# Optimization experiments

Hardware: AMD Instinct MI355X
Metric: run time of the kernel (lower is better)

Reference implementation:

```python
import jax, jax.numpy as jnp
import numpy as np
from jax import lax

N = 50000          # fluid particles
E = 1_600_000      # radius-graph edges (avg degree 32)
F_IN = 4           # fluidFeatures
NB = 8             # n = m = 8 basis functions per axis
K = NB * NB        # 64 total basis functions
SUPPORT = 1.0      # attributes['support']
LAYERS = [32, 64, 64, 2]


def setup_inputs() -> dict:
    key = jax.random.key(0)
    ks = jax.random.split(key, 24)
    inp = {
        "fluidPositions": jax.random.uniform(ks[0], (N, 2), jnp.float32),
        "fluidFeatures": jax.random.normal(ks[1], (N, F_IN), jnp.float32),
        "edge_i": jax.random.randint(ks[2], (E,), 0, N),  # receiver
        "edge_j": jax.random.randint(ks[3], (E,), 0, N),  # sender
    }
    # conv in/out channels per RbfNet wiring (boundaryFeatures == 0):
    dims = [(F_IN, LAYERS[0]), (2 * LAYERS[0], LAYERS[1]), (LAYERS[1], LAYERS[2]), (LAYERS[2], LAYERS[3])]
    k = 4
    for idx, (ci, co) in enumerate(dims):
        inp[f"cw{idx}"] = 0.1 * jax.random.normal(ks[k], (K, ci, co), jnp.float32); k += 1
        inp[f"cb{idx}"] = jnp.zeros((co,), jnp.float32)
        inp[f"fw{idx}"] = 0.1 * jax.random.normal(ks[k], (ci, co), jnp.float32); k += 1
        inp[f"fb{idx}"] = jnp.zeros((co,), jnp.float32)
    return inp


def _linear_basis(x, n):
    # hat (linear) RBF basis on n uniformly spaced centers in [-1, 1]
    centers = jnp.linspace(-1.0, 1.0, n, dtype=x.dtype)
    spacing = 2.0 / (n - 1)
    return jnp.maximum(0.0, 1.0 - jnp.abs(x[:, None] - centers[None, :]) / spacing)  # [E, n]


def _edge_basis(pos, ei, ej):
    # fluidEdgeLengths = -(pos[j] - pos[i]) / support, clamped to [-1, 1]
    d = (pos[ei] - pos[ej]) / SUPPORT
    d = jnp.clip(d, -1.0, 1.0)
    mask = ei != ej  # centerIgnore: drop self edges
    d = jnp.where(mask[:, None], d, jnp.array([1.0, 0.0], d.dtype))  # keep atan2 grads finite
    r = jnp.sqrt(jnp.sum(d * d, axis=-1) + 1e-12)
    u = jnp.clip(2.0 * r - 1.0, -1.0, 1.0)          # polar mapping: radius -> [-1, 1]
    v = jnp.arctan2(d[:, 1], d[:, 0]) / jnp.pi       # polar mapping: angle  -> [-1, 1]
    bu = _linear_basis(u, NB)
    bv = _linear_basis(v, NB)
    basis = (bu[:, :, None] * bv[:, None, :]).reshape(ei.shape[0], K)  # separable 2D basis
    return basis * mask[:, None].astype(basis.dtype)


def _rbf_conv(x, ei, ej, basis, W, b):
    # out[i] = sum_{e: dst(e)=i} sum_k basis[e,k] * (x[src(e)] @ W[k]) + b
    xj = x[ej]                           # [E, Cin] neighbor gather
    n_nodes = x.shape[0]
    init = jnp.zeros((n_nodes, W.shape[-1]), x.dtype)
    def body(acc, kw):
        bk, Wk = kw                      # bk: [E], Wk: [Cin, Cout]
        mom = jax.ops.segment_sum(bk[:, None] * xj, ei, num_segments=n_nodes)  # [N, Cin]
        return acc + mom @ Wk, None
    out, _ = lax.scan(body, init, (basis.T, W))
    return out + b


def reference(fluidPositions, fluidFeatures, edge_i, edge_j,
              cw0, cb0, fw0, fb0, cw1, cb1, fw1, fb1,
              cw2, cb2, fw2, fb2, cw3, cb3, fw3, fb3):
    basis = _edge_basis(fluidPositions, edge_i, edge_j)
    # layer 0: dense branch + fluid continuous conv, hstacked
    lin0 = fluidFeatures @ fw0 + fb0
    conv0 = _rbf_conv(fluidFeatures, edge_i, edge_j, basis, cw0, cb0)
    ans = jnp.concatenate([lin0, conv0], axis=1)  # [N, 64]
    # layer 1: features 32 != 64 -> no residual
    a = jax.nn.relu(ans)
    ans = _rbf_conv(a, edge_i, edge_j, basis, cw1, cb1) + a @ fw1 + fb1
    # layer 2: features 64 == 64 -> residual add
    a = jax.nn.relu(ans)
    ans = _rbf_conv(a, edge_i, edge_j, basis, cw2, cb2) + a @ fw2 + fb2 + ans
    # layer 3: features 64 != 2 -> no residual
    a = jax.nn.relu(ans)
    ans = _rbf_conv(a, edge_i, edge_j, basis, cw3, cb3) + a @ fw3 + fb3
    return ans / 128.0
```

## Files before the change

kernel.cpp:

```cpp
#include <hip/hip_runtime.h>
#include <math.h>

typedef _Float16 h8 __attribute__((ext_vector_type(8)));
typedef _Float16 h2 __attribute__((ext_vector_type(2)));
typedef float f32x4 __attribute__((ext_vector_type(4)));
typedef unsigned u32x2 __attribute__((ext_vector_type(2)));
typedef unsigned u32x4 __attribute__((ext_vector_type(4)));

__device__ __forceinline__ float clampf(float x, float lo, float hi) {
    return fminf(fmaxf(x, lo), hi);
}

__global__ void zero_ints(int* __restrict__ p, int n) {
    int i = blockIdx.x * 256 + threadIdx.x;
    if (i < n) p[i] = 0;
}

__global__ void repack_wh(const float* __restrict__ cw, const float* __restrict__ fw,
                          _Float16* __restrict__ Wh) {
    int idx = blockIdx.x * 256 + threadIdx.x;
    int total = 4 * 130 * 512;
    if (idx >= total) return;
    int j8 = idx & 7;
    int l = (idx >> 3) & 63;
    int rest = idx >> 9;
    int s = rest % 130;
    int t = rest / 130;
    int p = s * 32 + ((l >> 4) * 8) + j8;
    int co = t * 16 + (l & 15);
    float v = 0.f;
    if (p < 4096) {
        int tile = p >> 8;
        int g = (p >> 6) & 3;
        int m = (p >> 2) & 15;
        int i = p & 3;
        int mt = tile >> 2;
        int ct = tile & 3;
        int bin = mt * 16 + g * 4 + i;
        int c = ct * 16 + m;
        v = cw[(bin * 64 + c) * 64 + co];
    } else if (p < 4160) {
        v = fw[(p - 4096) * 64 + co];
    }
    Wh[idx] = (_Float16)v;
}

__global__ void repack_wh3(const float* __restrict__ cw, const float* __restrict__ fw,
                           _Float16* __restrict__ Wh) {
    int idx = blockIdx.x * 256 + threadIdx.x;
    int total = 130 * 512;
    if (idx >= total) return;
    int j8 = idx & 7;
    int l = (idx >> 3) & 63;
    int s = idx >> 9;
    int p = s * 32 + ((l >> 4) * 8) + j8;
    int co = l & 15;
    float v = 0.f;
    if (co < 2) {
        if (p < 4096) {
            int tile = p >> 8;
            int g = (p >> 6) & 3;
            int m = (p >> 2) & 15;
            int i = p & 3;
            int mt = tile >> 2;
            int ct = tile & 3;
            int bin = mt * 16 + g * 4 + i;
            int c = ct * 16 + m;
            v = cw[(bin * 64 + c) * 2 + co];
        } else if (p < 4160) {
            v = fw[(p - 4096) * 2 + co];
        }
    }
    Wh[idx] = (_Float16)v;
}

__global__ void repack_w0h(const float* __restrict__ cw0, const float* __restrict__ fw0,
                           _Float16* __restrict__ Wh) {
    int idx = blockIdx.x * 256 + threadIdx.x;
    int total = 4 * 9 * 512;
    if (idx >= total) return;
    int j8 = idx & 7;
    int l = (idx >> 3) & 63;
    int rest = idx >> 9;
    int s = rest % 9;
    int t = rest / 9;
    int p = s * 32 + ((l >> 4) * 8) + j8;
    int co = t * 16 + (l & 15);
    float v = 0.f;
    if (p < 256) {
        int bin = p & 63;
        int c = p >> 6;
        if (co >= 32) v = cw0[(bin * 4 + c) * 32 + (co - 32)];
    } else if (p < 260) {
        int c = p - 256;
        if (co < 32) v = fw0[c * 32 + co];
    }
    Wh[idx] = (_Float16)v;
}

__global__ void edge_hist(const int* __restrict__ ei, const int* __restrict__ ej,
                          int* __restrict__ counts, int E) {
    int e = blockIdx.x * 256 + threadIdx.x;
    if (e >= E) return;
    int i = ei[e], j = ej[e];
    if (i != j) atomicAdd(&counts[i], 1);
}

__global__ __launch_bounds__(1024) void scan_kernel(const int* __restrict__ counts,
                                                    int* __restrict__ offs,
                                                    int* __restrict__ cursor, int N) {
    __shared__ int sums[1024];
    const int t = threadIdx.x;
    const int per = (N + 1023) / 1024;
    const int lo = t * per;
    const int hi = min(lo + per, N);
    int s = 0;
    for (int i = lo; i < hi; ++i) s += counts[i];
    sums[t] = s;
    __syncthreads();
    for (int d = 1; d < 1024; d <<= 1) {
        int v = (t >= d) ? sums[t - d] : 0;
        __syncthreads();
        sums[t] += v;
        __syncthreads();
    }
    int run = (t > 0) ? sums[t - 1] : 0;
    for (int i = lo; i < hi; ++i) {
        offs[i] = run;
        cursor[i] = run;
        run += counts[i];
    }
    if (t == 1023) offs[N] = sums[1023];
}

__global__ void edge_scatter(const int* __restrict__ ei, const int* __restrict__ ej,
                             const float* __restrict__ pos, int* __restrict__ cursor,
                             uint4* __restrict__ csr_all, int E) {
    int e = blockIdx.x * 256 + threadIdx.x;
    if (e >= E) return;
    int i = ei[e], j = ej[e];
    if (i == j) return;
    float dx = clampf(pos[i * 2 + 0] - pos[j * 2 + 0], -1.f, 1.f);
    float dy = clampf(pos[i * 2 + 1] - pos[j * 2 + 1], -1.f, 1.f);
    float r = sqrtf(dx * dx + dy * dy + 1e-12f);
    float u = clampf(2.f * r - 1.f, -1.f, 1.f);
    float v = atan2f(dy, dx) * 0.3183098861837907f;
    float tu = (u + 1.f) * 3.5f;
    float tv = (v + 1.f) * 3.5f;
    int iu = min(6, max(0, (int)floorf(tu)));
    int iv = min(6, max(0, (int)floorf(tv)));
    float fu = clampf(tu - (float)iu, 0.f, 1.f);
    float fv = clampf(tv - (float)iv, 0.f, 1.f);
    bool even = (iu & 1) == 0;
    int rowi0 = even ? iu : iu + 1;
    int rowi1 = even ? iu + 1 : iu;
    float wu0 = even ? (1.f - fu) : fu;
    float wu1 = even ? fu : (1.f - fu);
    float gv = 1.f - fv;
    unsigned a0 = (unsigned)__builtin_bit_cast(unsigned short, (_Float16)(wu0 * gv)) |
                  ((unsigned)__builtin_bit_cast(unsigned short, (_Float16)(wu0 * fv)) << 16);
    unsigned a1 = (unsigned)__builtin_bit_cast(unsigned short, (_Float16)(wu1 * gv)) |
                  ((unsigned)__builtin_bit_cast(unsigned short, (_Float16)(wu1 * fv)) << 16);
    int p = atomicAdd(&cursor[i], 1);
    csr_all[p] = make_uint4(
        (unsigned)j | ((unsigned)(rowi0 >> 1) << 17) | ((unsigned)(rowi1 >> 1) << 19) |
            ((unsigned)iv << 21),
        0u, a0, a1);
}

__device__ __forceinline__ void mom_phase1_64(
    const _Float16* __restrict__ xh, const uint4* __restrict__ csr_all,
    _Float16* Ast, _Float16* Bst, unsigned bst_byte,
    int e0, int e1, int lane, f32x4* acc) {
    const int half = lane >> 5;
    const int el = lane & 31;
    const int q = lane >> 4;
    const int m = lane & 15;
    for (int bs = e0; bs < e1; bs += 32) {
        {
            uint4 z4 = make_uint4(0, 0, 0, 0);
#pragma unroll
            for (int zz = 0; zz < 4; ++zz) ((uint4*)Ast)[zz * 64 + lane] = z4;
        }
        int e = bs + el;
        bool ok = e < e1;
        uint4 ca = csr_all[ok ? e : e0];
        int jme = ok ? (int)(ca.x & 0x1FFFF) : -1;
        {
            int iv = (ca.x >> 21) & 7;
            int rowi = half ? (int)((((ca.x >> 19) & 3) << 1) + 1)
                            : (int)(((ca.x >> 17) & 3) << 1);
            h2 wts = __builtin_bit_cast(h2, half ? ca.w : ca.z);
            if (ok) {
                int bin0 = rowi * 8 + iv;
                int bin1 = bin0 + 1;
                int a0 = bin0 * 32 + (((el >> 3) + (bin0 >> 1)) & 3) * 8 + (el & 7);
                int a1 = bin1 * 32 + (((el >> 3) + (bin1 >> 1)) & 3) * 8 + (el & 7);
                Ast[a0] = wts[0];
                Ast[a1] = wts[1];
            }
        }
#pragma unroll
        for (int it = 0; it < 4; ++it) {
            int ee = it * 8 + (lane >> 3);
            int jj = __shfl(jme, ee);
            int c0 = (lane & 7) * 8;
            uint4 bv = make_uint4(0, 0, 0, 0);
            if (jj >= 0) bv = *(const uint4*)(xh + (size_t)jj * 64 + c0);
            int sub = (ee >> 2) * 4 + (c0 >> 4);
            ((uint4*)Bst)[sub * 8 + (ee & 3) * 2 + ((c0 >> 3) & 1)] = bv;
        }
        h8 af[4];
#pragma unroll
        for (int mt = 0; mt < 4; ++mt) {
            int binr = mt * 16 + m;
            int aoff = binr * 32 + ((q + (binr >> 1)) & 3) * 8;
            af[mt] = *(const h8*)(Ast + aoff);
        }
        unsigned bb = bst_byte + (unsigned)(q * 1024 + m * 8);
        h8 bf[4];
#pragma unroll
        for (int ct = 0; ct < 4; ++ct) {
            u32x2 lo, hi;
            asm volatile("ds_read_b64_tr_b16 %0, %2 offset:%3\n\t"
                         "ds_read_b64_tr_b16 %1, %2 offset:%4"
                         : "=&v"(lo), "=&v"(hi)
                         : "v"(bb), "i"(ct * 128), "i"(ct * 128 + 512)
                         : "memory");
            u32x4 t;
            t[0] = lo[0]; t[1] = lo[1]; t[2] = hi[0]; t[3] = hi[1];
            bf[ct] = __builtin_bit_cast(h8, t);
        }
        asm volatile("s_waitcnt lgkmcnt(0)" ::: "memory");
        __builtin_amdgcn_sched_barrier(0);
        __builtin_amdgcn_s_setprio(1);
#pragma unroll
        for (int mt = 0; mt < 4; ++mt)
#pragma unroll
            for (int ct = 0; ct < 4; ++ct)
                acc[mt * 4 + ct] = __builtin_amdgcn_mfma_f32_16x16x32_f16(
                    af[mt], bf[ct], acc[mt * 4 + ct], 0, 0, 0);
        __builtin_amdgcn_s_setprio(0);
    }
}

__device__ __forceinline__ void mom_writeback_64(const f32x4* acc, _Float16* momrow,
                                                 int lane) {
#pragma unroll
    for (int t = 0; t < 16; ++t) {
        h2 lo = {(_Float16)acc[t][0], (_Float16)acc[t][1]};
        h2 hi = {(_Float16)acc[t][2], (_Float16)acc[t][3]};
        h2* dst = (h2*)(momrow + t * 256 + (lane >> 4) * 64 + (lane & 15) * 4);
        dst[0] = lo;
        dst[1] = hi;
    }
}

template <int MODE>
__global__ __launch_bounds__(1024, 4) void conv64_mfma(
    const _Float16* __restrict__ xh, const float* __restrict__ x32,
    const _Float16* __restrict__ Wh,
    const float* __restrict__ cb, const float* __restrict__ fb,
    const int* __restrict__ offs, const uint4* __restrict__ csr_all,
    float* __restrict__ out32, _Float16* __restrict__ xh_out, int nNodes) {
    constexpr int TM = 16;
    constexpr int KSTEPS = 130;
    constexpr int RSH = 4184;
    extern __shared__ _Float16 smem[];
    const int tid = threadIdx.x;
    const int w = tid >> 6;
    const int lane = tid & 63;
    const int base = blockIdx.x * TM;
    const int n = base + w;

    _Float16* Ast = smem + w * RSH;
    _Float16* Bst = Ast + 2048;
    const unsigned bst_byte = (unsigned)((w * RSH + 2048) * 2);

    f32x4 acc[16] = {{0, 0, 0, 0}, {0, 0, 0, 0}, {0, 0, 0, 0}, {0, 0, 0, 0},
                     {0, 0, 0, 0}, {0, 0, 0, 0}, {0, 0, 0, 0}, {0, 0, 0, 0},
                     {0, 0, 0, 0}, {0, 0, 0, 0}, {0, 0, 0, 0}, {0, 0, 0, 0},
                     {0, 0, 0, 0}, {0, 0, 0, 0}, {0, 0, 0, 0}, {0, 0, 0, 0}};

    if (n < nNodes) {
        mom_phase1_64(xh, csr_all, Ast, Bst, bst_byte, offs[n], offs[n + 1], lane, acc);
        mom_writeback_64(acc, smem + w * RSH, lane);
        smem[w * RSH + 4096 + lane] = xh[(size_t)n * 64 + lane];
    }

    const int s0 = w * 8 + min(w, 2);
    const int s_end = s0 + 8 + (w < 2 ? 1 : 0);
    const int quad = lane >> 4;
    const _Float16* arow = smem + (lane & 15) * RSH;

    const uint4* Bp = (const uint4*)Wh;
    uint4 b0[4], b1[4];
#pragma unroll
    for (int t = 0; t < 4; ++t) {
        b0[t] = Bp[((size_t)t * KSTEPS + s0) * 64 + lane];
        b1[t] = Bp[((size_t)t * KSTEPS + s0 + 1) * 64 + lane];
    }
    __syncthreads();
    f32x4 acc2[4] = {{0, 0, 0, 0}, {0, 0, 0, 0}, {0, 0, 0, 0}, {0, 0, 0, 0}};
    for (int s = s0; s < s_end; ++s) {
        uint4 bq[4];
#pragma unroll
        for (int t = 0; t < 4; ++t) {
            bq[t] = b0[t];
            b0[t] = b1[t];
            if (s + 2 < s_end) b1[t] = Bp[((size_t)t * KSTEPS + s + 2) * 64 + lane];
        }
        h8 a = *(const h8*)(arow + s * 32 + quad * 8);
#pragma unroll
        for (int t = 0; t < 4; ++t)
            acc2[t] = __builtin_amdgcn_mfma_f32_16x16x32_f16(a, __builtin_bit_cast(h8, bq[t]),
                                                             acc2[t], 0, 0, 0);
    }
    __syncthreads();
    f32x4* red = (f32x4*)smem;
#pragma unroll
    for (int t = 0; t < 4; ++t) red[(w * 4 + t) * 64 + lane] = acc2[t];
    __syncthreads();
    if (w < 4) {
        f32x4 s = {0, 0, 0, 0};
#pragma unroll
        for (int g = 0; g < 16; ++g) s += red[(g * 4 + w) * 64 + lane];
        const int co = w * 16 + (lane & 15);
#pragma unroll
        for (int i = 0; i < 4; ++i) {
            int nn = base + quad * 4 + i;
            if (nn < nNodes) {
                float res = s[i] + cb[co] + fb[co];
                if (MODE == 2) res += x32[(size_t)nn * 64 + co];
                if (MODE == 1) out32[(size_t)nn * 64 + co] = res;
                xh_out[(size_t)nn * 64 + co] = (_Float16)fmaxf(res, 0.f);
            }
        }
    }
}

__global__ __launch_bounds__(1024, 4) void conv_last_mfma(
    const _Float16* __restrict__ xh, const _Float16* __restrict__ Wh3,
    const float* __restrict__ cb3, const float* __restrict__ fb3,
    const int* __restrict__ offs, const uint4* __restrict__ csr_all,
    float* __restrict__ out, int nNodes) {
    constexpr int TM = 16;
    constexpr int RSH = 4184;
    extern __shared__ _Float16 smem[];
    const int tid = threadIdx.x;
    const int w = tid >> 6;
    const int lane = tid & 63;
    const int base = blockIdx.x * TM;
    const int n = base + w;

    _Float16* Ast = smem + w * RSH;
    _Float16* Bst = Ast + 2048;
    const unsigned bst_byte = (unsigned)((w * RSH + 2048) * 2);

    f32x4 acc[16] = {{0, 0, 0, 0}, {0, 0, 0, 0}, {0, 0, 0, 0}, {0, 0, 0, 0},
                     {0, 0, 0, 0}, {0, 0, 0, 0}, {0, 0, 0, 0}, {0, 0, 0, 0},
                     {0, 0, 0, 0}, {0, 0, 0, 0}, {0, 0, 0, 0}, {0, 0, 0, 0},
                     {0, 0, 0, 0}, {0, 0, 0, 0}, {0, 0, 0, 0}, {0, 0, 0, 0}};

    if (n < nNodes) {
        mom_phase1_64(xh, csr_all, Ast, Bst, bst_byte, offs[n], offs[n + 1], lane, acc);
        mom_writeback_64(acc, smem + w * RSH, lane);
        smem[w * RSH + 4096 + lane] = xh[(size_t)n * 64 + lane];
    }

    const int s0 = w * 8 + min(w, 2);
    const int s_end = s0 + 8 + (w < 2 ? 1 : 0);
    const int quad = lane >> 4;
    const _Float16* arow = smem + (lane & 15) * RSH;
    const uint4* Bp = (const uint4*)Wh3;

    __syncthreads();
    f32x4 acc2 = {0, 0, 0, 0};
    for (int s = s0; s < s_end; ++s) {
        uint4 bq = Bp[(size_t)s * 64 + lane];
        h8 a = *(const h8*)(arow + s * 32 + quad * 8);
        acc2 = __builtin_amdgcn_mfma_f32_16x16x32_f16(a, __builtin_bit_cast(h8, bq),
                                                      acc2, 0, 0, 0);
    }
    __syncthreads();
    f32x4* red = (f32x4*)smem;
    red[w * 64 + lane] = acc2;
    __syncthreads();
    if (w == 0) {
        f32x4 s = {0, 0, 0, 0};
#pragma unroll
        for (int g = 0; g < 16; ++g) s += red[g * 64 + lane];
        const int co = lane & 15;
        if (co < 2) {
#pragma unroll
            for (int i = 0; i < 4; ++i) {
                int nn = base + quad * 4 + i;
                if (nn < nNodes)
                    out[nn * 2 + co] = (s[i] + cb3[co] + fb3[co]) * (1.f / 128.f);
            }
        }
    }
}

__global__ __launch_bounds__(1024, 4) void conv0_mfma(
    const float* __restrict__ xf, const _Float16* __restrict__ W0h,
    const float* __restrict__ cb0, const float* __restrict__ fb0,
    const int* __restrict__ offs, const uint4* __restrict__ csr_all,
    _Float16* __restrict__ xh_out, int nNodes) {
    constexpr int TM = 16;
    constexpr int RSH0 = 296;
    constexpr int MOMSZ = 16 * RSH0;
    extern __shared__ _Float16 smem[];
    const int tid = threadIdx.x;
    const int w = tid >> 6;
    const int lane = tid & 63;
    const int base = blockIdx.x * TM;
    const int n = base + w;

    _Float16* Ast = smem + MOMSZ + w * 2560;
    _Float16* Bst = Ast + 2048;
    _Float16* momrow = smem + w * RSH0;
    const unsigned bst_byte = (unsigned)((MOMSZ + w * 2560 + 2048) * 2);

    f32x4 acc[4] = {{0, 0, 0, 0}, {0, 0, 0, 0}, {0, 0, 0, 0}, {0, 0, 0, 0}};

    if (n < nNodes) {
        const int e0 = offs[n], e1 = offs[n + 1];
        const int half = lane >> 5;
        const int el = lane & 31;
        const int q = lane >> 4;
        const int m = lane & 15;
        for (int bs = e0; bs < e1; bs += 32) {
            {
                uint4 z4 = make_uint4(0, 0, 0, 0);
#pragma unroll
                for (int zz = 0; zz < 4; ++zz) ((uint4*)Ast)[zz * 64 + lane] = z4;
            }
            int e = bs + el;
            bool ok = e < e1;
            uint4 ca = csr_all[ok ? e : e0];
            int jme = ok ? (int)(ca.x & 0x1FFFF) : -1;
            {
                int iv = (ca.x >> 21) & 7;
                int rowi = half ? (int)((((ca.x >> 19) & 3) << 1) + 1)
                                : (int)(((ca.x >> 17) & 3) << 1);
                h2 wts = __builtin_bit_cast(h2, half ? ca.w : ca.z);
                if (ok) {
                    int bin0 = rowi * 8 + iv;
                    int bin1 = bin0 + 1;
                    int a0 = bin0 * 32 + (((el >> 3) + (bin0 >> 1)) & 3) * 8 + (el & 7);
                    int a1 = bin1 * 32 + (((el >> 3) + (bin1 >> 1)) & 3) * 8 + (el & 7);
                    Ast[a0] = wts[0];
                    Ast[a1] = wts[1];
                }
            }
            if (half == 0) {
                float4 xj = make_float4(0.f, 0.f, 0.f, 0.f);
                if (jme >= 0) xj = *(const float4*)(xf + (size_t)jme * 4);
                h2 d0 = {(_Float16)xj.x, (_Float16)xj.y};
                h2 d1 = {(_Float16)xj.z, (_Float16)xj.w};
                uint4 bv = make_uint4(__builtin_bit_cast(unsigned, d0),
                                      __builtin_bit_cast(unsigned, d1), 0u, 0u);
                uint4* dst = (uint4*)Bst + (el >> 2) * 8 + (el & 3) * 2;
                dst[0] = bv;
                dst[1] = make_uint4(0, 0, 0, 0);
            }
            h8 af[4];
#pragma unroll
            for (int mt = 0; mt < 4; ++mt) {
                int binr = mt * 16 + m;
                int aoff = binr * 32 + ((q + (binr >> 1)) & 3) * 8;
                af[mt] = *(const h8*)(Ast + aoff);
            }
            unsigned bb = bst_byte + (unsigned)(q * 256 + m * 8);
            u32x2 lo, hi;
            asm volatile("ds_read_b64_tr_b16 %0, %2 offset:0\n\t"
                         "ds_read_b64_tr_b16 %1, %2 offset:128"
                         : "=&v"(lo), "=&v"(hi)
                         : "v"(bb)
                         : "memory");
            u32x4 tt;
            tt[0] = lo[0]; tt[1] = lo[1]; tt[2] = hi[0]; tt[3] = hi[1];
            h8 b = __builtin_bit_cast(h8, tt);
            asm volatile("s_waitcnt lgkmcnt(0)" ::: "memory");
            __builtin_amdgcn_sched_barrier(0);
            __builtin_amdgcn_s_setprio(1);
#pragma unroll
            for (int mt = 0; mt < 4; ++mt)
                acc[mt] = __builtin_amdgcn_mfma_f32_16x16x32_f16(af[mt], b, acc[mt], 0, 0, 0);
            __builtin_amdgcn_s_setprio(0);
        }
        if ((lane & 15) < 4) {
#pragma unroll
            for (int mt = 0; mt < 4; ++mt) {
                _Float16* dst = momrow + mt * 16 + (lane >> 4) * 4 + 64 * (lane & 15);
                ((h2*)dst)[0] = h2{(_Float16)acc[mt][0], (_Float16)acc[mt][1]};
                ((h2*)dst)[1] = h2{(_Float16)acc[mt][2], (_Float16)acc[mt][3]};
            }
        }
        if (lane < 7) {
            h2 z = {(_Float16)0.f, (_Float16)0.f};
            h2* zp = (h2*)(momrow + 260 + lane * 4);
            zp[0] = z;
            zp[1] = z;
        }
        if (lane < 4) momrow[256 + lane] = (_Float16)xf[(size_t)n * 4 + lane];
    }

    const int quad = lane >> 4;
    const _Float16* arow = smem + (lane & 15) * RSH0;
    const uint4* Bp = (const uint4*)W0h;
    __syncthreads();
    f32x4 acc2[4] = {{0, 0, 0, 0}, {0, 0, 0, 0}, {0, 0, 0, 0}, {0, 0, 0, 0}};
    const int s0 = min(w, 9), s_end = min(w + 1, 9);
    for (int s = s0; s < s_end; ++s) {
        uint4 bq[4];
#pragma unroll
        for (int t = 0; t < 4; ++t) bq[t] = Bp[((size_t)t * 9 + s) * 64 + lane];
        h8 a = *(const h8*)(arow + s * 32 + quad * 8);
#pragma unroll
        for (int t = 0; t < 4; ++t)
            acc2[t] = __builtin_amdgcn_mfma_f32_16x16x32_f16(a, __builtin_bit_cast(h8, bq[t]),
                                                             acc2[t], 0, 0, 0);
    }
    __syncthreads();
    f32x4* red = (f32x4*)(smem + MOMSZ);
#pragma unroll
    for (int t = 0; t < 4; ++t) red[(w * 4 + t) * 64 + lane] = acc2[t];
    __syncthreads();
    if (w < 4) {
        f32x4 s = {0, 0, 0, 0};
#pragma unroll
        for (int g = 0; g < 16; ++g) s += red[(g * 4 + w) * 64 + lane];
        const int co = w * 16 + (lane & 15);
        const float bias = (co < 32) ? fb0[co] : cb0[co - 32];
#pragma unroll
        for (int i = 0; i < 4; ++i) {
            int nn = base + quad * 4 + i;
            if (nn < nNodes)
                xh_out[(size_t)nn * 64 + co] = (_Float16)fmaxf(s[i] + bias, 0.f);
        }
    }
}

extern "C" void kernel_launch(void* const* d_in, const int* in_sizes, int n_in,
                              void* d_out, int out_size, void* d_ws, size_t ws_size,
                              hipStream_t stream) {
    const float* pos = (const float*)d_in[0];
    const float* feat = (const float*)d_in[1];
    const int* ei = (const int*)d_in[2];
    const int* ej = (const int*)d_in[3];
    const float* cw0 = (const float*)d_in[4];
    const float* cb0 = (const float*)d_in[5];
    const float* fw0 = (const float*)d_in[6];
    const float* fb0 = (const float*)d_in[7];
    const float* cw1 = (const float*)d_in[8];
    const float* cb1 = (const float*)d_in[9];
    const float* fw1 = (const float*)d_in[10];
    const float* fb1 = (const float*)d_in[11];
    const float* cw2 = (const float*)d_in[12];
    const float* cb2 = (const float*)d_in[13];
    const float* fw2 = (const float*)d_in[14];
    const float* fb2 = (const float*)d_in[15];
    const float* cw3 = (const float*)d_in[16];
    const float* cb3 = (const float*)d_in[17];
    const float* fw3 = (const float*)d_in[18];
    const float* fb3 = (const float*)d_in[19];
    float* outp = (float*)d_out;

    const int N = in_sizes[0] / 2;
    const int E = in_sizes[2];

    char* wsp = (char*)d_ws;
    size_t off = 0;
    auto alloc = [&](size_t bytes) -> void* {
        void* p = wsp + off;
        off = (off + bytes + 255) & ~(size_t)255;
        return p;
    };
    int* counts = (int*)alloc((size_t)N * 4);
    int* offs = (int*)alloc((size_t)(N + 1) * 4);
    int* cursor = (int*)alloc((size_t)N * 4);
    uint4* csr_all = (uint4*)alloc((size_t)E * 16);
    float* ansB = (float*)alloc((size_t)N * 64 * 4);
    _Float16* xh0 = (_Float16*)alloc((size_t)N * 64 * 2);
    _Float16* xhB = (_Float16*)alloc((size_t)N * 64 * 2);
    _Float16* xhC = (_Float16*)alloc((size_t)N * 64 * 2);
    _Float16* Wh1 = (_Float16*)alloc((size_t)4 * 130 * 512 * 2);
    _Float16* Wh2 = (_Float16*)alloc((size_t)4 * 130 * 512 * 2);
    _Float16* Wh3 = (_Float16*)alloc((size_t)130 * 512 * 2);
    _Float16* W0h = (_Float16*)alloc((size_t)4 * 9 * 512 * 2);
    (void)ws_size;
    (void)n_in;
    (void)out_size;

    const int BIG_LDS = 16 * 4184 * 2;
    const int LDS0 = (16 * 296 + 16 * 2560) * 2;
    hipFuncSetAttribute((const void*)&conv64_mfma<1>,
                        hipFuncAttributeMaxDynamicSharedMemorySize, BIG_LDS);
    hipFuncSetAttribute((const void*)&conv64_mfma<2>,
                        hipFuncAttributeMaxDynamicSharedMemorySize, BIG_LDS);
    hipFuncSetAttribute((const void*)&conv_last_mfma,
                        hipFuncAttributeMaxDynamicSharedMemorySize, BIG_LDS);
    hipFuncSetAttribute((const void*)&conv0_mfma,
                        hipFuncAttributeMaxDynamicSharedMemorySize, LDS0);

    zero_ints<<<dim3((N + 255) / 256), dim3(256), 0, stream>>>(counts, N);
    const int RT = 4 * 130 * 512;
    repack_wh<<<dim3((RT + 255) / 256), dim3(256), 0, stream>>>(cw1, fw1, Wh1);
    repack_wh<<<dim3((RT + 255) / 256), dim3(256), 0, stream>>>(cw2, fw2, Wh2);
    repack_wh3<<<dim3((130 * 512 + 255) / 256), dim3(256), 0, stream>>>(cw3, fw3, Wh3);
    repack_w0h<<<dim3((4 * 9 * 512 + 255) / 256), dim3(256), 0, stream>>>(cw0, fw0, W0h);
    edge_hist<<<dim3((E + 255) / 256), dim3(256), 0, stream>>>(ei, ej, counts, E);
    scan_kernel<<<dim3(1), dim3(1024), 0, stream>>>(counts, offs, cursor, N);
    edge_scatter<<<dim3((E + 255) / 256), dim3(256), 0, stream>>>(ei, ej, pos, cursor, csr_all, E);

    const int nb = (N + 15) / 16;
    conv0_mfma<<<dim3(nb), dim3(1024), LDS0, stream>>>(
        feat, W0h, cb0, fb0, offs, csr_all, xh0, N);
    conv64_mfma<1><<<dim3(nb), dim3(1024), BIG_LDS, stream>>>(
        xh0, (const float*)nullptr, Wh1, cb1, fb1, offs, csr_all, ansB, xhB, N);
    conv64_mfma<2><<<dim3(nb), dim3(1024), BIG_LDS, stream>>>(
        xhB, ansB, Wh2, cb2, fb2, offs, csr_all, (float*)nullptr, xhC, N);
    conv_last_mfma<<<dim3(nb), dim3(1024), BIG_LDS, stream>>>(
        xhC, Wh3, cb3, fb3, offs, csr_all, outp, N);
}
```

Baseline: 833.2 us.

## Software-pipeline CSR and neighbor feature gathers across edge batches in moment phase

Restructures the per-warp edge loop so that the CSR entry for two batches ahead and the neighbor feature rows for the next batch are loaded before the current batch's LDS staging and MFMA work. This is meant to hide global gather latency behind compute instead of stalling each iteration on dependent loads. In exchange it uses more registers (extra uint4 buffers), which may reduce occupancy under the 1024-thread launch bounds, and it issues prefetch loads past the batch range that are clamped to e0.

```diff
diff --git a/kernel.cpp b/kernel.cpp
--- a/kernel.cpp
+++ b/kernel.cpp
@@ -176,16 +176,47 @@
     const int el = lane & 31;
     const int q = lane >> 4;
     const int m = lane & 15;
+
+    bool ok = (e0 + el) < e1;
+    uint4 ca = csr_all[ok ? e0 + el : e0];
+    uint4 bv[4];
+    {
+        int jme = ok ? (int)(ca.x & 0x1FFFF) : -1;
+#pragma unroll
+        for (int it = 0; it < 4; ++it) {
+            int ee = it * 8 + (lane >> 3);
+            int jj = __shfl(jme, ee);
+            int c0 = (lane & 7) * 8;
+            uint4 t = make_uint4(0, 0, 0, 0);
+            if (jj >= 0) t = *(const uint4*)(xh + (size_t)jj * 64 + c0);
+            bv[it] = t;
+        }
+    }
+    bool okn = (e0 + 32 + el) < e1;
+    uint4 ca_n = csr_all[okn ? e0 + 32 + el : e0];
+
     for (int bs = e0; bs < e1; bs += 32) {
+        uint4 bv_n[4];
+        {
+            int jme_n = okn ? (int)(ca_n.x & 0x1FFFF) : -1;
+#pragma unroll
+            for (int it = 0; it < 4; ++it) {
+                int ee = it * 8 + (lane >> 3);
+                int jj = __shfl(jme_n, ee);
+                int c0 = (lane & 7) * 8;
+                uint4 t = make_uint4(0, 0, 0, 0);
+                if (jj >= 0) t = *(const uint4*)(xh + (size_t)jj * 64 + c0);
+                bv_n[it] = t;
+            }
+        }
+        bool oknn = (bs + 64 + el) < e1;
+        uint4 ca_nn = csr_all[oknn ? bs + 64 + el : e0];
+
         {
             uint4 z4 = make_uint4(0, 0, 0, 0);
 #pragma unroll
             for (int zz = 0; zz < 4; ++zz) ((uint4*)Ast)[zz * 64 + lane] = z4;
         }
-        int e = bs + el;
-        bool ok = e < e1;
-        uint4 ca = csr_all[ok ? e : e0];
-        int jme = ok ? (int)(ca.x & 0x1FFFF) : -1;
         {
             int iv = (ca.x >> 21) & 7;
             int rowi = half ? (int)((((ca.x >> 19) & 3) << 1) + 1)
@@ -203,12 +234,9 @@
 #pragma unroll
         for (int it = 0; it < 4; ++it) {
             int ee = it * 8 + (lane >> 3);
-            int jj = __shfl(jme, ee);
             int c0 = (lane & 7) * 8;
-            uint4 bv = make_uint4(0, 0, 0, 0);
-            if (jj >= 0) bv = *(const uint4*)(xh + (size_t)jj * 64 + c0);
             int sub = (ee >> 2) * 4 + (c0 >> 4);
-            ((uint4*)Bst)[sub * 8 + (ee & 3) * 2 + ((c0 >> 3) & 1)] = bv;
+            ((uint4*)Bst)[sub * 8 + (ee & 3) * 2 + ((c0 >> 3) & 1)] = bv[it];
         }
         h8 af[4];
 #pragma unroll
@@ -241,6 +269,13 @@
                 acc[mt * 4 + ct] = __builtin_amdgcn_mfma_f32_16x16x32_f16(
                     af[mt], bf[ct], acc[mt * 4 + ct], 0, 0, 0);
         __builtin_amdgcn_s_setprio(0);
+
+        ok = okn;
+        ca = ca_n;
+        okn = oknn;
+        ca_n = ca_nn;
+#pragma unroll
+        for (int it = 0; it < 4; ++it) bv[it] = bv_n[it];
     }
 }
 
```

Result: slower. 1.062 ms (+27.5%).
